# Kernel tuning notes

Measured on AMD Instinct MI355X. Metric: run time of the kernel, lower is better.

Reference implementation:

```python
import jax, jax.numpy as jnp
import numpy as np
import math

B, T, D, H, K = 4, 2048, 1024, 16, 64

def setup_inputs() -> dict:
    key = jax.random.key(0)
    ks = jax.random.split(key, 6)
    scale = 1.0 / math.sqrt(D)  # keep logits in a sane range (torch code uses raw randn params)
    X = jax.random.normal(ks[0], (B, T, D), dtype=jnp.float32)
    Wq = jax.random.normal(ks[1], (H, D, K), dtype=jnp.float32) * scale
    Wk = jax.random.normal(ks[2], (H, D, K), dtype=jnp.float32) * scale
    Wv = jax.random.normal(ks[3], (H, D, K), dtype=jnp.float32) * scale
    Wo = jax.random.normal(ks[4], (H * K, H * K), dtype=jnp.float32) * (1.0 / math.sqrt(H * K))
    bo = jnp.zeros((H * K,), dtype=jnp.float32)
    return {"X": X, "Wq": Wq, "Wk": Wk, "Wv": Wv, "Wo": Wo, "bo": bo}

def reference(X, Wq, Wk, Wv, Wo, bo):
    # per-head projections: [B,H,T,K]
    q = jnp.einsum('btc,nck->bntk', X, Wq)
    k = jnp.einsum('btc,nck->bntk', X, Wk)
    v = jnp.einsum('btc,nck->bntk', X, Wv)
    # full score matrix [B,H,T,T] with causal mask (query t attends to s <= t)
    scores = jnp.einsum('bntk,bnsk->bnts', q, k) / math.sqrt(K)
    causal = jnp.tril(jnp.ones((T, T), dtype=bool))
    scores = jnp.where(causal[None, None], scores, jnp.finfo(scores.dtype).min)
    attn = jax.nn.softmax(scores, axis=-1)
    out = jnp.einsum('bnts,bnsk->bntk', attn, v)  # [B,H,T,K]
    # concat heads along feature dim (head-major ordering, matches torch.cat over heads)
    out = jnp.transpose(out, (0, 2, 1, 3)).reshape(B, T, H * K)
    # output projection (torch nn.Linear: x @ W.T + b)
    return out @ Wo.T + bo
```

## Files before the change

### kernel.cpp

```cpp
#include <hip/hip_runtime.h>
#include <hip/hip_bf16.h>
#include <math.h>

#define B_SZ 4
#define T_SZ 2048
#define D_SZ 1024
#define H_SZ 16
#define K_SZ 64

typedef __attribute__((ext_vector_type(8))) short bf8_t;
typedef __attribute__((ext_vector_type(4))) float f4_t;

__device__ __forceinline__ ushort f2bf(float f) {
    union { float f; unsigned u; } v; v.f = f;
    return (ushort)((v.u + 0x7fffu + ((v.u >> 16) & 1u)) >> 16);
}

__device__ __forceinline__ uint cvt_pk_bf16(float lo, float hi) {
    uint r;
    asm("v_cvt_pk_bf16_f32 %0, %1, %2" : "=v"(r) : "v"(lo), "v"(hi));
    return r;
}

__device__ __forceinline__ void gld_lds16(const ushort* g, ushort* l) {
    __builtin_amdgcn_global_load_lds(
        (const __attribute__((address_space(1))) void*)g,
        (__attribute__((address_space(3))) void*)l, 16, 0, 0);
}

#define Q_PRESCALE 0.18033688011112042f

__global__ __launch_bounds__(256) void convert_bf16_kernel(
    const float* __restrict__ src, ushort* __restrict__ dst)
{
    const size_t i = ((size_t)blockIdx.x * 256 + threadIdx.x) * 8;
    float4 a = *(const float4*)(src + i);
    float4 b = *(const float4*)(src + i + 4);
    ushort o[8] = {f2bf(a.x), f2bf(a.y), f2bf(a.z), f2bf(a.w),
                   f2bf(b.x), f2bf(b.y), f2bf(b.z), f2bf(b.w)};
    *(uint4*)(dst + i) = *(const uint4*)o;
}

__global__ __launch_bounds__(256) void transpose_w_kernel(
    const float* __restrict__ Wq, const float* __restrict__ Wk,
    const float* __restrict__ Wv, ushort* __restrict__ WT)
{
    __shared__ __align__(16) float tile[64][68];
    const int tid = threadIdx.x;
    const int d0  = blockIdx.x * 64;
    const int g   = blockIdx.y;
    const int sel = g >> 4, h = g & 15;
    const float* W = (sel == 0 ? Wq : (sel == 1 ? Wk : Wv)) + (size_t)h * D_SZ * K_SZ;

    {
        const int r = tid >> 2, ks = (tid & 3) * 16;
        const float4* src = (const float4*)(W + (size_t)(d0 + r) * 64 + ks);
        float4* dst = (float4*)&tile[r][ks];
        dst[0] = src[0]; dst[1] = src[1]; dst[2] = src[2]; dst[3] = src[3];
    }
    __syncthreads();
    {
        const int k = tid >> 2, ds = (tid & 3) * 16;
        ushort o[16];
        #pragma unroll
        for (int i = 0; i < 16; ++i) o[i] = f2bf(tile[ds + i][k]);
        uint4* dst = (uint4*)&WT[(size_t)(sel * 1024 + h * 64 + k) * 1024 + d0 + ds];
        dst[0] = ((const uint4*)o)[0];
        dst[1] = ((const uint4*)o)[1];
    }
}

__device__ __forceinline__ void gemm_bt_tile(
    const ushort* __restrict__ A, const ushort* __restrict__ Bt,
    int Kdim, int m0, int n0, ushort* As, ushort* Bs, f4_t acc[4][4])
{
    const int tid  = threadIdx.x;
    const int lane = tid & 63, wv = tid >> 6;
    const int l16  = lane & 15, quad = lane >> 4;
    const int wm   = (wv >> 1) * 64, wn = (wv & 1) * 64;
    const int sw   = (l16 >> 1) & 3;

    const int ra0 = tid >> 2,         qa0 = (tid & 3) ^ ((ra0 >> 1) & 3);
    const int ra1 = (tid + 256) >> 2, qa1 = (tid & 3) ^ ((ra1 >> 1) & 3);
    ushort* ldsA0 = As + (size_t)(wv * 64) * 8;
    ushort* ldsA1 = As + (size_t)(wv * 64 + 256) * 8;
    ushort* ldsB0 = Bs + (size_t)(wv * 64) * 8;
    ushort* ldsB1 = Bs + (size_t)(wv * 64 + 256) * 8;
    const ushort* gA0 = A  + (size_t)(m0 + ra0) * Kdim + qa0 * 8;
    const ushort* gA1 = A  + (size_t)(m0 + ra1) * Kdim + qa1 * 8;
    const ushort* gB0 = Bt + (size_t)(n0 + ra0) * Kdim + qa0 * 8;
    const ushort* gB1 = Bt + (size_t)(n0 + ra1) * Kdim + qa1 * 8;

    for (int k0 = 0; k0 < Kdim; k0 += 32) {
        __syncthreads();
        gld_lds16(gA0 + k0, ldsA0);
        gld_lds16(gA1 + k0, ldsA1);
        gld_lds16(gB0 + k0, ldsB0);
        gld_lds16(gB1 + k0, ldsB1);
        __syncthreads();

        bf8_t a[4], b[4];
        #pragma unroll
        for (int mt = 0; mt < 4; ++mt)
            a[mt] = *(const bf8_t*)&As[(wm + mt * 16 + l16) * 32 + ((quad ^ sw) * 8)];
        #pragma unroll
        for (int nt = 0; nt < 4; ++nt)
            b[nt] = *(const bf8_t*)&Bs[(wn + nt * 16 + l16) * 32 + ((quad ^ sw) * 8)];
        #pragma unroll
        for (int mt = 0; mt < 4; ++mt)
            #pragma unroll
            for (int nt = 0; nt < 4; ++nt)
                acc[mt][nt] = __builtin_amdgcn_mfma_f32_16x16x32_bf16(
                    a[mt], b[nt], acc[mt][nt], 0, 0, 0);
    }
}

__global__ __launch_bounds__(256) void gemm_qkv_kernel(
    const ushort* __restrict__ Xb, const ushort* __restrict__ WT,
    ushort* __restrict__ Qo, ushort* __restrict__ Ko, ushort* __restrict__ Vto)
{
    __shared__ __align__(16) ushort As[128 * 32];
    __shared__ __align__(16) ushort Bs[128 * 32];
    const int n0 = blockIdx.x * 128, m0 = blockIdx.y * 128;

    f4_t acc[4][4];
    #pragma unroll
    for (int i = 0; i < 4; ++i)
        #pragma unroll
        for (int j = 0; j < 4; ++j) acc[i][j] = (f4_t){0.f, 0.f, 0.f, 0.f};

    gemm_bt_tile(Xb, WT, 1024, m0, n0, As, Bs, acc);

    const int tid = threadIdx.x;
    const int lane = tid & 63, wv = tid >> 6;
    const int l16 = lane & 15, quad = lane >> 4;
    const int wm = (wv >> 1) * 64, wn = (wv & 1) * 64;
    const int sel = n0 >> 10;

    if (sel < 2) {
        ushort* Out = (sel == 0 ? Qo : Ko);
        const float osc = (sel == 0) ? Q_PRESCALE : 1.0f;
        #pragma unroll
        for (int nt = 0; nt < 4; ++nt) {
            const int col = n0 + wn + nt * 16 + l16;
            const int h = (col >> 6) & 15, kk = col & 63;
            #pragma unroll
            for (int mt = 0; mt < 4; ++mt) {
                #pragma unroll
                for (int r = 0; r < 4; ++r) {
                    const int row = m0 + wm + mt * 16 + quad * 4 + r;
                    const int bb = row >> 11, t = row & 2047;
                    Out[((size_t)(bb * 16 + h) * 2048 + t) * 64 + kk] =
                        f2bf(acc[mt][nt][r] * osc);
                }
            }
        }
    } else {
        #pragma unroll
        for (int nt = 0; nt < 4; ++nt) {
            const int col = n0 + wn + nt * 16 + l16;
            const int h = (col >> 6) & 15, kk = col & 63;
            #pragma unroll
            for (int mt = 0; mt < 4; ++mt) {
                const int base = m0 + wm + mt * 16 + quad * 4;
                const int bb = base >> 11, t = base & 2047;
                ushort o4[4];
                #pragma unroll
                for (int r = 0; r < 4; ++r) o4[r] = f2bf(acc[mt][nt][r]);
                *(uint2*)&Vto[((size_t)(bb * 16 + h) * 64 + kk) * 2048 + t] =
                    *(const uint2*)o4;
            }
        }
    }
}

__global__ __launch_bounds__(256) void gemm_out_kernel(
    const ushort* __restrict__ Yb, const ushort* __restrict__ WoB,
    const float* __restrict__ bo, float* __restrict__ Out)
{
    __shared__ __align__(16) ushort As[128 * 32];
    __shared__ __align__(16) ushort Bs[128 * 32];
    const int n0 = blockIdx.x * 128, m0 = blockIdx.y * 128;

    f4_t acc[4][4];
    #pragma unroll
    for (int i = 0; i < 4; ++i)
        #pragma unroll
        for (int j = 0; j < 4; ++j) acc[i][j] = (f4_t){0.f, 0.f, 0.f, 0.f};

    gemm_bt_tile(Yb, WoB, 1024, m0, n0, As, Bs, acc);

    const int tid = threadIdx.x;
    const int lane = tid & 63, wv = tid >> 6;
    const int l16 = lane & 15, quad = lane >> 4;
    const int wm = (wv >> 1) * 64, wn = (wv & 1) * 64;

    #pragma unroll
    for (int nt = 0; nt < 4; ++nt) {
        const int col = n0 + wn + nt * 16 + l16;
        const float bias = bo[col];
        #pragma unroll
        for (int mt = 0; mt < 4; ++mt) {
            #pragma unroll
            for (int r = 0; r < 4; ++r) {
                const int row = m0 + wm + mt * 16 + quad * 4 + r;
                Out[(size_t)row * 1024 + col] = acc[mt][nt][r] + bias;
            }
        }
    }
}

__global__ __launch_bounds__(64, 2) void attn_mfma_kernel(
    const ushort* __restrict__ Qg, const ushort* __restrict__ Kg,
    const ushort* __restrict__ Vtg, ushort* __restrict__ Y)
{
    __shared__ __align__(16) ushort Ph[2][32 * 72];

    const int lane = threadIdx.x;
    const int l16  = lane & 15;
    const int quad = lane >> 4;

    const int lin = blockIdx.x;
    const int xcd = lin & 7;
    const int idx = lin >> 3;
    const int bh  = xcd * 8 + (idx & 7);
    const int jp  = idx >> 3;
    const int bb  = bh >> 4, h = bh & 15;

    const int trowL = jp * 32;
    const int trowH = (63 - jp) * 32;

    const ushort* Kbh = Kg  + (size_t)bh * T_SZ * K_SZ;
    const ushort* Vbh = Vtg + (size_t)bh * K_SZ * T_SZ;

    bf8_t qaL[2][2], qaH[2][2];
    #pragma unroll
    for (int mt = 0; mt < 2; ++mt) {
        const ushort* qpL = Qg + ((size_t)bh * T_SZ + trowL + mt * 16 + l16) * K_SZ + quad * 8;
        const ushort* qpH = Qg + ((size_t)bh * T_SZ + trowH + mt * 16 + l16) * K_SZ + quad * 8;
        qaL[mt][0] = *(const bf8_t*)qpL;
        qaL[mt][1] = *(const bf8_t*)(qpL + 32);
        qaH[mt][0] = *(const bf8_t*)qpH;
        qaH[mt][1] = *(const bf8_t*)(qpH + 32);
    }

    f4_t OL[2][4], OH[2][4];
    float lpL[2] = {0.f, 0.f}, lpH[2] = {0.f, 0.f};
    #pragma unroll
    for (int mt = 0; mt < 2; ++mt)
        #pragma unroll
        for (int dt = 0; dt < 4; ++dt) {
            OL[mt][dt] = (f4_t){0.f, 0.f, 0.f, 0.f};
            OH[mt][dt] = (f4_t){0.f, 0.f, 0.f, 0.f};
        }

    const int n_it = (trowH + 32 + 63) >> 6;

    bf8_t kb[4][2], vb[4][2];
    #pragma unroll
    for (int nt = 0; nt < 4; ++nt)
        #pragma unroll
        for (int hh = 0; hh < 2; ++hh) {
            kb[nt][hh] = *(const bf8_t*)&Kbh[(size_t)(nt * 16 + l16) * K_SZ + hh * 32 + quad * 8];
            vb[nt][hh] = *(const bf8_t*)&Vbh[(size_t)(nt * 16 + l16) * T_SZ + hh * 32 + quad * 8];
        }

    auto qk = [&](const bf8_t (&qa)[2][2], f4_t (&S)[4][2]) {
        #pragma unroll
        for (int nt = 0; nt < 4; ++nt)
            #pragma unroll
            for (int mt = 0; mt < 2; ++mt) {
                S[nt][mt] = (f4_t){0.f, 0.f, 0.f, 0.f};
                S[nt][mt] = __builtin_amdgcn_mfma_f32_16x16x32_bf16(
                    kb[nt][0], qa[mt][0], S[nt][mt], 0, 0, 0);
                S[nt][mt] = __builtin_amdgcn_mfma_f32_16x16x32_bf16(
                    kb[nt][1], qa[mt][1], S[nt][mt], 0, 0, 0);
            }
    };

    auto sm_pv = [&](f4_t (&S)[4][2], f4_t (&O)[2][4], float (&lp)[2],
                     int trow, ushort* myP, int s0) {
        const bool diag = (s0 + 64 > trow);

        #pragma unroll
        for (int mt = 0; mt < 2; ++mt) {
            const int qg = trow + mt * 16 + l16;
            #pragma unroll
            for (int nt = 0; nt < 4; ++nt) {
                float p[4];
                if (diag) {
                    #pragma unroll
                    for (int r = 0; r < 4; ++r) {
                        float x = S[nt][mt][r];
                        if (s0 + nt * 16 + quad * 4 + r > qg) x = -1e30f;
                        p[r] = __builtin_amdgcn_exp2f(x);
                    }
                } else {
                    #pragma unroll
                    for (int r = 0; r < 4; ++r)
                        p[r] = __builtin_amdgcn_exp2f(S[nt][mt][r]);
                }
                lp[mt] += (p[0] + p[1]) + (p[2] + p[3]);
                uint2 pk;
                pk.x = cvt_pk_bf16(p[0], p[1]);
                pk.y = cvt_pk_bf16(p[2], p[3]);
                *(uint2*)&myP[(mt * 16 + l16) * 72 + nt * 16 + quad * 4] = pk;
            }
        }
        asm volatile("" ::: "memory");
        bf8_t pa[2][2];
        #pragma unroll
        for (int mt = 0; mt < 2; ++mt) {
            const ushort* pr = &myP[(mt * 16 + l16) * 72];
            pa[mt][0] = *(const bf8_t*)(pr + quad * 8);
            pa[mt][1] = *(const bf8_t*)(pr + 32 + quad * 8);
        }
        asm volatile("" ::: "memory");

        #pragma unroll
        for (int dt = 0; dt < 4; ++dt)
            #pragma unroll
            for (int mt = 0; mt < 2; ++mt) {
                O[mt][dt] = __builtin_amdgcn_mfma_f32_16x16x32_bf16(
                    pa[mt][0], vb[dt][0], O[mt][dt], 0, 0, 0);
                O[mt][dt] = __builtin_amdgcn_mfma_f32_16x16x32_bf16(
                    pa[mt][1], vb[dt][1], O[mt][dt], 0, 0, 0);
            }
    };

    for (int it = 0; it < n_it; ++it) {
        const int s0 = it * 64;
        const bool doL  = (s0 < trowL + 32);
        const bool more = (it + 1 < n_it);
        const int  sn   = s0 + 64;

        f4_t S[4][2];

        qk(qaH, S);
        sm_pv(S, OH, lpH, trowH, Ph[0], s0);

        if (doL) qk(qaL, S);

        if (more) {
            #pragma unroll
            for (int nt = 0; nt < 4; ++nt)
                #pragma unroll
                for (int hh = 0; hh < 2; ++hh)
                    kb[nt][hh] = *(const bf8_t*)&Kbh[
                        (size_t)(sn + nt * 16 + l16) * K_SZ + hh * 32 + quad * 8];
        }

        if (doL) sm_pv(S, OL, lpL, trowL, Ph[1], s0);

        if (more) {
            #pragma unroll
            for (int nt = 0; nt < 4; ++nt)
                #pragma unroll
                for (int hh = 0; hh < 2; ++hh)
                    vb[nt][hh] = *(const bf8_t*)&Vbh[
                        (size_t)(nt * 16 + l16) * T_SZ + sn + hh * 32 + quad * 8];
        }
    }

    auto epilogue = [&](f4_t (&O)[2][4], float (&lp)[2], int trow) {
        #pragma unroll
        for (int mt = 0; mt < 2; ++mt) {
            float s = lp[mt];
            s += __shfl_xor(s, 16);
            s += __shfl_xor(s, 32);
            const float inv = 1.f / s;
            float invr[4];
            #pragma unroll
            for (int r = 0; r < 4; ++r)
                invr[r] = __shfl(inv, quad * 4 + r);
            #pragma unroll
            for (int dt = 0; dt < 4; ++dt) {
                const int col = h * 64 + dt * 16 + l16;
                #pragma unroll
                for (int r = 0; r < 4; ++r) {
                    const int tg = trow + mt * 16 + quad * 4 + r;
                    Y[((size_t)(bb * T_SZ + tg)) * (H_SZ * K_SZ) + col] =
                        f2bf(O[mt][dt][r] * invr[r]);
                }
            }
        }
    };
    epilogue(OH, lpH, trowH);
    epilogue(OL, lpL, trowL);
}

extern "C" void kernel_launch(void* const* d_in, const int* in_sizes, int n_in,
                              void* d_out, int out_size, void* d_ws, size_t ws_size,
                              hipStream_t stream) {
    const float* X  = (const float*)d_in[0];
    const float* Wq = (const float*)d_in[1];
    const float* Wk = (const float*)d_in[2];
    const float* Wv = (const float*)d_in[3];
    const float* Wo = (const float*)d_in[4];
    const float* bo = (const float*)d_in[5];
    float* out = (float*)d_out;

    const size_t NE = (size_t)B_SZ * H_SZ * T_SZ * K_SZ;
    ushort* Qb   = (ushort*)d_ws;
    ushort* Kb   = Qb + NE;
    ushort* Vb   = Kb + NE;
    ushort* Vtb  = Vb + NE;
    ushort* Yb   = Vtb + NE;
    ushort* Xb   = Yb + NE;
    ushort* WT   = Xb + NE;
    ushort* WoB  = WT + (size_t)3072 * 1024;

    convert_bf16_kernel<<<dim3(4096), 256, 0, stream>>>(X, Xb);
    convert_bf16_kernel<<<dim3(512), 256, 0, stream>>>(Wo, WoB);
    transpose_w_kernel<<<dim3(16, 48), 256, 0, stream>>>(Wq, Wk, Wv, WT);
    gemm_qkv_kernel<<<dim3(24, 64), 256, 0, stream>>>(Xb, WT, Qb, Kb, Vtb);
    attn_mfma_kernel<<<dim3(2048), 64, 0, stream>>>(Qb, Kb, Vtb, Yb);
    gemm_out_kernel<<<dim3(8, 64), 256, 0, stream>>>(Yb, WoB, bo, out);
}
```

Before: 302.3 us.

## Merge convert launches, swizzle GEMM blocks, add setprio, interleave attention QK

```diff
diff --git a/kernel.cpp b/kernel.cpp
--- a/kernel.cpp
+++ b/kernel.cpp
@@ -31,13 +31,17 @@
 #define Q_PRESCALE 0.18033688011112042f
 
 __global__ __launch_bounds__(256) void convert_bf16_kernel(
-    const float* __restrict__ src, ushort* __restrict__ dst)
-{
-    const size_t i = ((size_t)blockIdx.x * 256 + threadIdx.x) * 8;
+    const float* __restrict__ X, ushort* __restrict__ Xd,
+    const float* __restrict__ W, ushort* __restrict__ Wd)
+{
+    const int b = blockIdx.x;
+    const float* src;  ushort* dst;  size_t i;
+    if (b < 4096) { src = X; dst = Xd; i = ((size_t)b * 256 + threadIdx.x) * 8; }
+    else          { src = W; dst = Wd; i = ((size_t)(b - 4096) * 256 + threadIdx.x) * 8; }
     float4 a = *(const float4*)(src + i);
-    float4 b = *(const float4*)(src + i + 4);
+    float4 c = *(const float4*)(src + i + 4);
     ushort o[8] = {f2bf(a.x), f2bf(a.y), f2bf(a.z), f2bf(a.w),
-                   f2bf(b.x), f2bf(b.y), f2bf(b.z), f2bf(b.w)};
+                   f2bf(c.x), f2bf(c.y), f2bf(c.z), f2bf(c.w)};
     *(uint4*)(dst + i) = *(const uint4*)o;
 }
 
@@ -106,12 +110,14 @@
         #pragma unroll
         for (int nt = 0; nt < 4; ++nt)
             b[nt] = *(const bf8_t*)&Bs[(wn + nt * 16 + l16) * 32 + ((quad ^ sw) * 8)];
+        __builtin_amdgcn_s_setprio(1);
         #pragma unroll
         for (int mt = 0; mt < 4; ++mt)
             #pragma unroll
             for (int nt = 0; nt < 4; ++nt)
                 acc[mt][nt] = __builtin_amdgcn_mfma_f32_16x16x32_bf16(
                     a[mt], b[nt], acc[mt][nt], 0, 0, 0);
+        __builtin_amdgcn_s_setprio(0);
     }
 }
 
@@ -121,7 +127,9 @@
 {
     __shared__ __align__(16) ushort As[128 * 32];
     __shared__ __align__(16) ushort Bs[128 * 32];
-    const int n0 = blockIdx.x * 128, m0 = blockIdx.y * 128;
+    const int b   = blockIdx.x;
+    const int swz = (b & 7) * 192 + (b >> 3);
+    const int n0  = (swz % 24) * 128, m0 = (swz / 24) * 128;
 
     f4_t acc[4][4];
     #pragma unroll
@@ -180,7 +188,9 @@
 {
     __shared__ __align__(16) ushort As[128 * 32];
     __shared__ __align__(16) ushort Bs[128 * 32];
-    const int n0 = blockIdx.x * 128, m0 = blockIdx.y * 128;
+    const int b   = blockIdx.x;
+    const int swz = (b & 7) * 64 + (b >> 3);
+    const int n0  = (swz % 8) * 128, m0 = (swz / 8) * 128;
 
     f4_t acc[4][4];
     #pragma unroll
@@ -266,6 +276,7 @@
         }
 
     auto qk = [&](const bf8_t (&qa)[2][2], f4_t (&S)[4][2]) {
+        __builtin_amdgcn_s_setprio(1);
         #pragma unroll
         for (int nt = 0; nt < 4; ++nt)
             #pragma unroll
@@ -276,6 +287,7 @@
                 S[nt][mt] = __builtin_amdgcn_mfma_f32_16x16x32_bf16(
                     kb[nt][1], qa[mt][1], S[nt][mt], 0, 0, 0);
             }
+        __builtin_amdgcn_s_setprio(0);
     };
 
     auto sm_pv = [&](f4_t (&S)[4][2], f4_t (&O)[2][4], float (&lp)[2],
@@ -317,6 +329,7 @@
         }
         asm volatile("" ::: "memory");
 
+        __builtin_amdgcn_s_setprio(1);
         #pragma unroll
         for (int dt = 0; dt < 4; ++dt)
             #pragma unroll
@@ -326,6 +339,7 @@
                 O[mt][dt] = __builtin_amdgcn_mfma_f32_16x16x32_bf16(
                     pa[mt][1], vb[dt][1], O[mt][dt], 0, 0, 0);
             }
+        __builtin_amdgcn_s_setprio(0);
     };
 
     for (int it = 0; it < n_it; ++it) {
@@ -334,12 +348,10 @@
         const bool more = (it + 1 < n_it);
         const int  sn   = s0 + 64;
 
-        f4_t S[4][2];
-
-        qk(qaH, S);
-        sm_pv(S, OH, lpH, trowH, Ph[0], s0);
-
-        if (doL) qk(qaL, S);
+        f4_t SH[4][2], SL[4][2];
+
+        qk(qaH, SH);
+        if (doL) qk(qaL, SL);
 
         if (more) {
             #pragma unroll
@@ -350,7 +362,8 @@
                         (size_t)(sn + nt * 16 + l16) * K_SZ + hh * 32 + quad * 8];
         }
 
-        if (doL) sm_pv(S, OL, lpL, trowL, Ph[1], s0);
+        sm_pv(SH, OH, lpH, trowH, Ph[0], s0);
+        if (doL) sm_pv(SL, OL, lpL, trowL, Ph[1], s0);
 
         if (more) {
             #pragma unroll
@@ -410,10 +423,9 @@
     ushort* WT   = Xb + NE;
     ushort* WoB  = WT + (size_t)3072 * 1024;
 
-    convert_bf16_kernel<<<dim3(4096), 256, 0, stream>>>(X, Xb);
-    convert_bf16_kernel<<<dim3(512), 256, 0, stream>>>(Wo, WoB);
+    convert_bf16_kernel<<<dim3(4608), 256, 0, stream>>>(X, Xb, Wo, WoB);
     transpose_w_kernel<<<dim3(16, 48), 256, 0, stream>>>(Wq, Wk, Wv, WT);
-    gemm_qkv_kernel<<<dim3(24, 64), 256, 0, stream>>>(Xb, WT, Qb, Kb, Vtb);
+    gemm_qkv_kernel<<<dim3(1536), 256, 0, stream>>>(Xb, WT, Qb, Kb, Vtb);
     attn_mfma_kernel<<<dim3(2048), 64, 0, stream>>>(Qb, Kb, Vtb, Yb);
-    gemm_out_kernel<<<dim3(8, 64), 256, 0, stream>>>(Yb, WoB, bo, out);
-}
+    gemm_out_kernel<<<dim3(512), 256, 0, stream>>>(Yb, WoB, bo, out);
+}
```

Measured after the change: 306.4 us. No clear change (+1.3%).
